# Performance work log

Hardware: AMD Instinct MI355X
Metric: run time of the kernel (lower is better)

Reference implementation:

```python
import jax, jax.numpy as jnp
import numpy as np

H = 1024
W = 1024
SAMPLES_PER_SEG = 32
SIGMA_AA = 1.0
EDGE_CHUNK = 32  # matches torch chunk_size


def sample_bezier_path(control_points):
    # control_points: [N, 2], N = 3*S + 1 cubic segments
    N = control_points.shape[0]
    S = (N - 1) // 3
    idx = 3 * jnp.arange(S)
    p0 = control_points[idx][:, None, :]      # [S,1,2]
    p1 = control_points[idx + 1][:, None, :]
    p2 = control_points[idx + 2][:, None, :]
    p3 = control_points[idx + 3][:, None, :]
    t = jnp.linspace(0.0, 1.0, SAMPLES_PER_SEG, dtype=control_points.dtype)[None, :, None]  # [1,T,1]
    mt = 1.0 - t
    pts = (mt * mt * mt) * p0 + 3.0 * (mt * mt) * t * p1 + 3.0 * mt * (t * t) * p2 + (t * t * t) * p3
    return pts.reshape(S * SAMPLES_PER_SEG, 2)  # [M,2]


def compute_winding(path_points, sigma):
    # path_points: [M,2]; closed polygon edges (j -> (j+1)%M)
    M = path_points.shape[0]
    nxt = jnp.roll(path_points, -1, axis=0)
    x0, y0 = path_points[:, 0], path_points[:, 1]
    x1, y1 = nxt[:, 0], nxt[:, 1]
    dy = y1 - y0
    dx = x1 - x0
    # edges with |dy| < 1e-6 are skipped in the original (continue) -> zero contribution
    coeff = jnp.sign(dy) * (jnp.abs(dy) >= 1e-6).astype(path_points.dtype)
    grid_y = jnp.arange(H, dtype=path_points.dtype)  # rows
    grid_x = jnp.arange(W, dtype=path_points.dtype)  # cols

    n_chunks = M // EDGE_CHUNK
    def chunk_it(a):
        return a.reshape(n_chunks, EDGE_CHUNK)

    def body(acc, c):
        cx0, cy0, cdy, cdx, cc = c  # each [CH]
        t_cross = (grid_y[None, :] - cy0[:, None]) / (cdy[:, None] + 1e-8)          # [CH,H]
        x_cross = cx0[:, None] + t_cross * cdx[:, None]                              # [CH,H]
        valid_t = jax.nn.sigmoid(t_cross * 20.0) * jax.nn.sigmoid((1.0 - t_cross) * 20.0)  # [CH,H]
        crosses = jax.nn.sigmoid((x_cross[:, :, None] - grid_x[None, None, :]) / sigma)    # [CH,H,W]
        contrib = jnp.sum(crosses * (valid_t * cc[:, None])[:, :, None], axis=0)           # [H,W]
        return acc + contrib, None

    init = jnp.zeros((H, W), dtype=path_points.dtype)
    winding, _ = jax.lax.scan(body, init, (chunk_it(x0), chunk_it(y0), chunk_it(dy), chunk_it(dx), chunk_it(coeff)))
    return winding


def setup_inputs() -> dict:
    key = jax.random.key(0)
    k1, k2 = jax.random.split(key)
    control_points = jax.random.uniform(k1, (49, 2), dtype=jnp.float32) * jnp.float32(W)
    color = jax.random.uniform(k2, (3,), dtype=jnp.float32)
    return {"control_points": control_points, "color": color}


def reference(control_points, color):
    pts = sample_bezier_path(control_points)          # [M,2]
    winding = compute_winding(pts, SIGMA_AA)          # [H,W]
    alpha = jax.nn.sigmoid(winding * 4.0)             # [H,W]
    rgb = jnp.broadcast_to(color[None, None, :], (H, W, 3))
    rgba = jnp.concatenate([rgb, alpha[..., None]], axis=-1)  # [H,W,4]
    return rgba
```

## Files before the change

kernel.cpp:

```cpp
#include <hip/hip_runtime.h>

#define HH 1024
#define WW 1024
#define NPTS 512
#define W_EPS 1e-6f
#define CAP 64

__device__ __forceinline__ float sigmoidf(float z) {
    float e = __expf(-z);
    return __builtin_amdgcn_rcpf(1.0f + e);
}

__global__ __launch_bounds__(256) void render_kernel(
    const float* __restrict__ cp,
    const float* __restrict__ color,
    float* __restrict__ out)
{
    __shared__ float2 pts[NPTS];
    __shared__ float2 actXW[NPTS];
    __shared__ int    actTmin[NPTS];
    __shared__ int    actTmax[NPTS];
    __shared__ float2 bucket[16][CAP];
    __shared__ int    cnt[16];
    __shared__ float  satW[16];
    __shared__ int    n_act;

    const int tid = threadIdx.x;
    const int y = blockIdx.x;
    const float yf = (float)y;

    if (tid == 0) n_act = 0;
    if (tid < 16) cnt[tid] = 0;

    for (int i = tid; i < NPTS; i += 256) {
        int seg = i >> 5;
        int j = i & 31;
        float t = (float)j / 31.0f;
        float mt = 1.0f - t;
        int bb = 3 * seg * 2;
        float p0x = cp[bb + 0], p0y = cp[bb + 1];
        float p1x = cp[bb + 2], p1y = cp[bb + 3];
        float p2x = cp[bb + 4], p2y = cp[bb + 5];
        float p3x = cp[bb + 6], p3y = cp[bb + 7];
        float a0 = mt * mt * mt;
        float a1 = 3.0f * mt * mt * t;
        float a2 = 3.0f * mt * t * t;
        float a3 = t * t * t;
        pts[i] = make_float2(a0 * p0x + a1 * p1x + a2 * p2x + a3 * p3x,
                             a0 * p0y + a1 * p1y + a2 * p2y + a3 * p3y);
    }
    __syncthreads();

    for (int e = tid; e < NPTS; e += 256) {
        float2 p = pts[e];
        float2 q = pts[(e + 1) & (NPTS - 1)];
        float dy = q.y - p.y;
        float dx = q.x - p.x;
        float c = (dy > 0.0f) ? 1.0f : ((dy < 0.0f) ? -1.0f : 0.0f);
        if (fabsf(dy) < 1e-6f) c = 0.0f;
        float t = (yf - p.y) / (dy + 1e-8f);
        float vt = sigmoidf(t * 20.0f) * sigmoidf((1.0f - t) * 20.0f);
        float w = vt * c;
        if (fabsf(w) > W_EPS) {
            float xc = p.x + t * dx;
            int tmin = (int)ceilf((xc - 77.0f) * 0.015625f);
            if (tmin < 0) tmin = 0;
            if (tmin > 16) tmin = 16;
            int tmax = (int)floorf((xc + 14.0f) * 0.015625f);
            if (tmax > 15) tmax = 15;
            int idx = atomicAdd(&n_act, 1);
            actXW[idx] = make_float2(xc, w);
            actTmin[idx] = tmin;
            actTmax[idx] = tmax;
            for (int tt = tmin; tt <= tmax; ++tt) {
                int pos = atomicAdd(&cnt[tt], 1);
                if (pos < CAP) bucket[tt][pos] = make_float2(xc, w);
            }
        }
    }
    __syncthreads();

    const int n = n_act;

    {
        int grp = tid >> 4;
        int l16 = tid & 15;
        float partial = 0.0f;
        for (int i = l16; i < n; i += 16)
            if (grp < actTmin[i]) partial += actXW[i].y;
        partial += __shfl_down(partial, 8, 16);
        partial += __shfl_down(partial, 4, 16);
        partial += __shfl_down(partial, 2, 16);
        partial += __shfl_down(partial, 1, 16);
        if (l16 == 0) satW[grp] = partial;
    }
    __syncthreads();

    const float cr = color[0], cg = color[1], cb = color[2];
    const int wv = tid >> 6;
    const int lane = tid & 63;
    float4* orow = ((float4*)out) + y * WW;

    for (int k = 0; k < 4; ++k) {
        const int t = k * 4 + wv;
        const int x = t * 64 + lane;
        const float xf = (float)x;
        float acc;
        const int m = cnt[t];
        if (m <= CAP) {
            acc = satW[t];
            for (int j = 0; j < m; ++j) {
                float2 d = bucket[t][j];
                acc = fmaf(d.y, sigmoidf(d.x - xf), acc);
            }
        } else {
            acc = 0.0f;
            for (int i = 0; i < n; ++i) {
                int tmin = actTmin[i];
                if (t < tmin) {
                    acc += actXW[i].y;
                } else if (t <= actTmax[i]) {
                    float2 d = actXW[i];
                    acc = fmaf(d.y, sigmoidf(d.x - xf), acc);
                }
            }
        }
        orow[x] = make_float4(cr, cg, cb, sigmoidf(4.0f * acc));
    }
}

extern "C" void kernel_launch(void* const* d_in, const int* in_sizes, int n_in,
                              void* d_out, int out_size, void* d_ws, size_t ws_size,
                              hipStream_t stream) {
    const float* cp = (const float*)d_in[0];
    const float* color = (const float*)d_in[1];
    float* out = (float*)d_out;
    render_kernel<<<HH, 256, 0, stream>>>(cp, color, out);
}
```

Before: 64.56 us.

## Use one thread per pixel with 1024-thread blocks and recompute Bezier points inline

Each block now runs 1024 threads, so each thread produces exactly one output pixel instead of looping over four tiles. The Bezier samples are recomputed per edge from control points cached in shared memory, which removes the points array and one barrier. Each wave computes its own saturated-weight prefix with a full-wave xor reduction, replacing the shared satW pass and another barrier. The per-tile bucket capacity is halved to shrink shared memory, which risks falling back to the slow full-scan path more often. Larger blocks may also lower scheduling flexibility.

New measurement: 65.76 us. Within noise of the previous version (+1.9%).

```diff
diff --git a/kernel.cpp b/kernel.cpp
--- a/kernel.cpp
+++ b/kernel.cpp
@@ -3,75 +3,73 @@
 #define HH 1024
 #define WW 1024
 #define NPTS 512
+#define TPB 1024
 #define W_EPS 1e-6f
-#define CAP 64
+#define CAP 32
 
 __device__ __forceinline__ float sigmoidf(float z) {
     float e = __expf(-z);
     return __builtin_amdgcn_rcpf(1.0f + e);
 }
 
-__global__ __launch_bounds__(256) void render_kernel(
+__device__ __forceinline__ float2 bez(const float* cpL, int i) {
+    i &= (NPTS - 1);
+    int seg = i >> 5;
+    int j = i & 31;
+    float t = (float)j * (1.0f / 31.0f);
+    float mt = 1.0f - t;
+    int b = 6 * seg;
+    float a0 = mt * mt * mt;
+    float a1 = 3.0f * mt * mt * t;
+    float a2 = 3.0f * mt * t * t;
+    float a3 = t * t * t;
+    return make_float2(
+        a0 * cpL[b+0] + a1 * cpL[b+2] + a2 * cpL[b+4] + a3 * cpL[b+6],
+        a0 * cpL[b+1] + a1 * cpL[b+3] + a2 * cpL[b+5] + a3 * cpL[b+7]);
+}
+
+__global__ __launch_bounds__(TPB) void render_kernel(
     const float* __restrict__ cp,
     const float* __restrict__ color,
     float* __restrict__ out)
 {
-    __shared__ float2 pts[NPTS];
+    __shared__ float  cpL[98];
+    __shared__ float  colL[3];
     __shared__ float2 actXW[NPTS];
-    __shared__ int    actTmin[NPTS];
-    __shared__ int    actTmax[NPTS];
+    __shared__ int    actTMM[NPTS];
     __shared__ float2 bucket[16][CAP];
     __shared__ int    cnt[16];
-    __shared__ float  satW[16];
     __shared__ int    n_act;
 
     const int tid = threadIdx.x;
     const int y = blockIdx.x;
     const float yf = (float)y;
 
+    if (tid < 98) cpL[tid] = cp[tid];
+    if (tid < 3)  colL[tid] = color[tid];
     if (tid == 0) n_act = 0;
     if (tid < 16) cnt[tid] = 0;
-
-    for (int i = tid; i < NPTS; i += 256) {
-        int seg = i >> 5;
-        int j = i & 31;
-        float t = (float)j / 31.0f;
-        float mt = 1.0f - t;
-        int bb = 3 * seg * 2;
-        float p0x = cp[bb + 0], p0y = cp[bb + 1];
-        float p1x = cp[bb + 2], p1y = cp[bb + 3];
-        float p2x = cp[bb + 4], p2y = cp[bb + 5];
-        float p3x = cp[bb + 6], p3y = cp[bb + 7];
-        float a0 = mt * mt * mt;
-        float a1 = 3.0f * mt * mt * t;
-        float a2 = 3.0f * mt * t * t;
-        float a3 = t * t * t;
-        pts[i] = make_float2(a0 * p0x + a1 * p1x + a2 * p2x + a3 * p3x,
-                             a0 * p0y + a1 * p1y + a2 * p2y + a3 * p3y);
-    }
     __syncthreads();
 
-    for (int e = tid; e < NPTS; e += 256) {
-        float2 p = pts[e];
-        float2 q = pts[(e + 1) & (NPTS - 1)];
+    if (tid < NPTS) {
+        float2 p = bez(cpL, tid);
+        float2 q = bez(cpL, tid + 1);
         float dy = q.y - p.y;
         float dx = q.x - p.x;
         float c = (dy > 0.0f) ? 1.0f : ((dy < 0.0f) ? -1.0f : 0.0f);
         if (fabsf(dy) < 1e-6f) c = 0.0f;
-        float t = (yf - p.y) / (dy + 1e-8f);
+        float t = (yf - p.y) * __builtin_amdgcn_rcpf(dy + 1e-8f);
         float vt = sigmoidf(t * 20.0f) * sigmoidf((1.0f - t) * 20.0f);
         float w = vt * c;
         if (fabsf(w) > W_EPS) {
-            float xc = p.x + t * dx;
+            float xc = fmaf(t, dx, p.x);
             int tmin = (int)ceilf((xc - 77.0f) * 0.015625f);
-            if (tmin < 0) tmin = 0;
-            if (tmin > 16) tmin = 16;
+            tmin = max(0, min(16, tmin));
             int tmax = (int)floorf((xc + 14.0f) * 0.015625f);
-            if (tmax > 15) tmax = 15;
+            tmax = max(-1, min(15, tmax));
             int idx = atomicAdd(&n_act, 1);
             actXW[idx] = make_float2(xc, w);
-            actTmin[idx] = tmin;
-            actTmax[idx] = tmax;
+            actTMM[idx] = tmin | ((tmax + 1) << 8);
             for (int tt = tmin; tt <= tmax; ++tt) {
                 int pos = atomicAdd(&cnt[tt], 1);
                 if (pos < CAP) bucket[tt][pos] = make_float2(xc, w);
@@ -80,53 +78,44 @@
     }
     __syncthreads();
 
+    const int t = tid >> 6;
+    const int lane = tid & 63;
     const int n = n_act;
+    const float xf = (float)(t * 64 + lane);
 
-    {
-        int grp = tid >> 4;
-        int l16 = tid & 15;
-        float partial = 0.0f;
-        for (int i = l16; i < n; i += 16)
-            if (grp < actTmin[i]) partial += actXW[i].y;
-        partial += __shfl_down(partial, 8, 16);
-        partial += __shfl_down(partial, 4, 16);
-        partial += __shfl_down(partial, 2, 16);
-        partial += __shfl_down(partial, 1, 16);
-        if (l16 == 0) satW[grp] = partial;
+    float sat = 0.0f;
+    for (int i = lane; i < n; i += 64) {
+        int tmin = actTMM[i] & 0xff;
+        if (t < tmin) sat += actXW[i].y;
     }
-    __syncthreads();
+    #pragma unroll
+    for (int o = 32; o > 0; o >>= 1) sat += __shfl_xor(sat, o);
 
-    const float cr = color[0], cg = color[1], cb = color[2];
-    const int wv = tid >> 6;
-    const int lane = tid & 63;
-    float4* orow = ((float4*)out) + y * WW;
-
-    for (int k = 0; k < 4; ++k) {
-        const int t = k * 4 + wv;
-        const int x = t * 64 + lane;
-        const float xf = (float)x;
-        float acc;
-        const int m = cnt[t];
-        if (m <= CAP) {
-            acc = satW[t];
-            for (int j = 0; j < m; ++j) {
-                float2 d = bucket[t][j];
+    float acc;
+    const int m = cnt[t];
+    if (m <= CAP) {
+        acc = sat;
+        for (int j = 0; j < m; ++j) {
+            float2 d = bucket[t][j];
+            acc = fmaf(d.y, sigmoidf(d.x - xf), acc);
+        }
+    } else {
+        acc = 0.0f;
+        for (int i = 0; i < n; ++i) {
+            int tmm = actTMM[i];
+            int tmin = tmm & 0xff;
+            int tmax = (tmm >> 8) - 1;
+            if (t < tmin) {
+                acc += actXW[i].y;
+            } else if (t <= tmax) {
+                float2 d = actXW[i];
                 acc = fmaf(d.y, sigmoidf(d.x - xf), acc);
             }
-        } else {
-            acc = 0.0f;
-            for (int i = 0; i < n; ++i) {
-                int tmin = actTmin[i];
-                if (t < tmin) {
-                    acc += actXW[i].y;
-                } else if (t <= actTmax[i]) {
-                    float2 d = actXW[i];
-                    acc = fmaf(d.y, sigmoidf(d.x - xf), acc);
-                }
-            }
         }
-        orow[x] = make_float4(cr, cg, cb, sigmoidf(4.0f * acc));
     }
+
+    float4* orow = ((float4*)out) + y * WW;
+    orow[tid] = make_float4(colL[0], colL[1], colL[2], sigmoidf(4.0f * acc));
 }
 
 extern "C" void kernel_launch(void* const* d_in, const int* in_sizes, int n_in,
@@ -135,5 +124,5 @@
     const float* cp = (const float*)d_in[0];
     const float* color = (const float*)d_in[1];
     float* out = (float*)d_out;
-    render_kernel<<<HH, 256, 0, stream>>>(cp, color, out);
+    render_kernel<<<HH, TPB, 0, stream>>>(cp, color, out);
 }
```
